# Performance work log

Measured on AMD Instinct MI355X. Metric: run time of the kernel, lower is better.

The kernel has to match this reference:

```python
import jax, jax.numpy as jnp
import numpy as np

B, N, C, K = 16, 1024, 192, 9
H = 4 * C  # hidden of second MLP pair


def _gelu(x):
    return jax.nn.gelu(x, approximate=False)  # torch nn.GELU default is exact erf


def _mlp(x, w1, b1, w2, b2):
    # TwoLayerNN: Linear -> GELU -> Linear
    return _gelu(x @ w1.T + b1) @ w2.T + b2


def _linear_init(key, out_d, in_d):
    k1, k2 = jax.random.split(key)
    s = 1.0 / np.sqrt(in_d)
    w = jax.random.uniform(k1, (out_d, in_d), minval=-s, maxval=s, dtype=jnp.float32)
    b = jax.random.uniform(k2, (out_d,), minval=-s, maxval=s, dtype=jnp.float32)
    return w, b


def setup_inputs() -> dict:
    key = jax.random.key(0)
    ks = jax.random.split(key, 10)
    x = jax.random.normal(ks[0], (B, N, C), dtype=jnp.float32)
    il1_w1, il1_b1 = _linear_init(ks[1], C, C)
    il1_w2, il1_b2 = _linear_init(ks[2], C, C)
    ol1_w1, ol1_b1 = _linear_init(ks[3], C, C)
    ol1_w2, ol1_b2 = _linear_init(ks[4], C, C)
    il2_w1, il2_b1 = _linear_init(ks[5], H, C)
    il2_w2, il2_b2 = _linear_init(ks[6], C, H)
    ol2_w1, ol2_b1 = _linear_init(ks[7], H, C)
    ol2_w2, ol2_b2 = _linear_init(ks[8], C, H)
    fc_w, fc_b = _linear_init(ks[9], C, 2 * C)  # Conv1d(2C, C, 1) == Linear(2C->C)
    return dict(x=x,
                il1_w1=il1_w1, il1_b1=il1_b1, il1_w2=il1_w2, il1_b2=il1_b2,
                fc_w=fc_w, fc_b=fc_b,
                ol1_w1=ol1_w1, ol1_b1=ol1_b1, ol1_w2=ol1_w2, ol1_b2=ol1_b2,
                il2_w1=il2_w1, il2_b1=il2_b1, il2_w2=il2_w2, il2_b2=il2_b2,
                ol2_w1=ol2_w1, ol2_b1=ol2_b1, ol2_w2=ol2_w2, ol2_b2=ol2_b2)


def reference(x, il1_w1, il1_b1, il1_w2, il1_b2, fc_w, fc_b,
              ol1_w1, ol1_b1, ol1_w2, ol1_b2,
              il2_w1, il2_b1, il2_w2, il2_b2,
              ol2_w1, ol2_b1, ol2_w2, ol2_b2):
    Bx, Nx, Cx = x.shape
    # 1) dense similarity + KNN graph (indices only; no grad path through sim)
    sim = jnp.einsum('bnc,bmc->bnm', x, x)                       # [B,N,N]
    _, graph = jax.lax.top_k(sim, K)                             # [B,N,K] int32
    shortcut = x
    # 2) node transform then gather-max aggregation
    h = _mlp(x.reshape(Bx * Nx, Cx), il1_w1, il1_b1, il1_w2, il1_b2).reshape(Bx, Nx, Cx)
    nb = jnp.take_along_axis(h[:, None, :, :], graph[:, :, :, None], axis=2)  # [B,N,K,C]
    agg = jnp.max(nb - h[:, :, None, :], axis=2)                 # [B,N,C]
    # 3) stack along new last dim then flatten -> interleaved channels [x_c0,agg_c0,x_c1,...]
    cat = jnp.stack([h, agg], axis=-1).reshape(Bx, Nx, 2 * Cx)   # [B,N,2C]
    h = cat @ fc_w.T + fc_b                                      # Conv1d k=1 == Linear
    h = _mlp(_gelu(h).reshape(Bx * Nx, Cx), ol1_w1, ol1_b1, ol1_w2, ol1_b2).reshape(Bx, Nx, Cx)
    x1 = h + shortcut
    # 4) FFN block (two TwoLayerNNs with external GELU between them)
    f = _mlp(x1.reshape(Bx * Nx, Cx), il2_w1, il2_b1, il2_w2, il2_b2)
    f = _mlp(_gelu(f), ol2_w1, ol2_b1, ol2_w2, ol2_b2).reshape(Bx, Nx, Cx)
    return f + x1
```

## Files before the change

### kernel.cpp

```cpp
#include <hip/hip_runtime.h>
#include <hip/hip_bf16.h>
#include <math.h>

#define DEVINL __device__ __forceinline__

typedef __attribute__((ext_vector_type(4))) float f32x4;
typedef __attribute__((ext_vector_type(8))) short s16x8;

DEVINL unsigned short f2bf(float f) {
  union { float f; unsigned u; } v; v.f = f;
  unsigned r = v.u + 0x7FFFu + ((v.u >> 16) & 1u);
  return (unsigned short)(r >> 16);
}
DEVINL float bf2f(unsigned short s) {
  union { unsigned u; float f; } v; v.u = ((unsigned)s) << 16;
  return v.f;
}
DEVINL float gelu_exact(float x) {
  return 0.5f * x * (1.0f + erff(x * 0.70710678118654752f));
}

__global__ __launch_bounds__(256) void conv_kernel(const float* __restrict__ x,
                                                   unsigned short* __restrict__ xh,
                                                   unsigned short* __restrict__ xl) {
  int i = blockIdx.x * 256 + threadIdx.x;
  float4 v = ((const float4*)x)[i];
  float f[4] = {v.x, v.y, v.z, v.w};
  unsigned short h[4], l[4];
#pragma unroll
  for (int j = 0; j < 4; ++j) {
    h[j] = f2bf(f[j]);
    l[j] = f2bf(f[j] - bf2f(h[j]));
  }
  uint2 uh, ul;
  uh.x = (unsigned)h[0] | ((unsigned)h[1] << 16);
  uh.y = (unsigned)h[2] | ((unsigned)h[3] << 16);
  ul.x = (unsigned)l[0] | ((unsigned)l[1] << 16);
  ul.y = (unsigned)l[2] | ((unsigned)l[3] << 16);
  ((uint2*)xh)[i] = uh;
  ((uint2*)xl)[i] = ul;
}

struct WArgs {
  const float* s[9];
  unsigned short* d[9];
  int n4[9];
};
__global__ __launch_bounds__(256) void wconv_kernel(WArgs a) {
  int seg = blockIdx.y;
  int i = blockIdx.x * 256 + threadIdx.x;
  if (i >= a.n4[seg]) return;
  float4 v = ((const float4*)a.s[seg])[i];
  float f[4] = {v.x, v.y, v.z, v.w};
  uint2 u;
  u.x = (unsigned)f2bf(f[0]) | ((unsigned)f2bf(f[1]) << 16);
  u.y = (unsigned)f2bf(f[2]) | ((unsigned)f2bf(f[3]) << 16);
  ((uint2*)a.d[seg])[i] = u;
}

__global__ __launch_bounds__(512)
#if __has_attribute(amdgpu_waves_per_eu)
__attribute__((amdgpu_waves_per_eu(2, 2)))
#endif
void simtopk_kernel(const unsigned short* __restrict__ xh,
                    const unsigned short* __restrict__ xl,
                    int* __restrict__ graph) {
  const int tid  = threadIdx.x;
  const int lane = tid & 63;
  const int w    = tid >> 6;
  const int wm   = w >> 1, wn = w & 1;

  const int lin  = blockIdx.y * 16 + blockIdx.x;
  const int work = (lin & 7) * 32 + (lin >> 3);
  const int rb   = work & 15;
  const int b    = work >> 4;

  extern __shared__ char smem[];
  float* Lv = (float*)smem;
  int*   Li = (int*)(smem + 20480);
  float* Mv = (float*)(smem + 40960);
  int*   Mi = (int*)(smem + 51200);

  const unsigned short* xhb = xh + (size_t)b * (1024 * 192);
  const unsigned short* xlb = xl + (size_t)b * (1024 * 192);

  s16x8 ah[6], al[6];
#pragma unroll
  for (int ks = 0; ks < 6; ++ks) {
    int r = rb * 64 + wm * 16 + (lane & 15);
    size_t off = (size_t)r * 192 + ks * 32 + (lane >> 4) * 8;
    ah[ks] = *(const s16x8*)(xhb + off);
    al[ks] = *(const s16x8*)(xlb + off);
  }

  auto stage = [&](int buf, int ct) {
    unsigned short* bH = (unsigned short*)(smem + buf * 49152);
    unsigned short* bL = bH + 12288;
#pragma unroll
    for (int i = 0; i < 3; ++i) {
      int c = tid + i * 512;
      int row = c / 24, cc = c - row * 24;
      size_t goff = (size_t)(ct * 64 + row) * 192 + (size_t)((cc ^ (row & 7)) * 8);
      __builtin_amdgcn_global_load_lds((const __attribute__((address_space(1))) void*)(xhb + goff),
                                       (__attribute__((address_space(3))) void*)(bH + (size_t)c * 8), 16, 0, 0);
      __builtin_amdgcn_global_load_lds((const __attribute__((address_space(1))) void*)(xlb + goff),
                                       (__attribute__((address_space(3))) void*)(bL + (size_t)c * 8), 16, 0, 0);
    }
  };

  float tv[9]; int tix[9];
#pragma unroll
  for (int k = 0; k < 9; ++k) { tv[k] = -3.0e38f; tix[k] = 1 << 30; }

  stage(0, 0);
  __syncthreads();

  int cur = 0;
  for (int ct = 0; ct < 16; ++ct) {
    if (ct < 15) stage(cur ^ 1, ct + 1);

    const unsigned short* bH = (const unsigned short*)(smem + cur * 49152);
    const unsigned short* bL = bH + 12288;

    f32x4 a0[2], a1[2], a2[2];
#pragma unroll
    for (int n2 = 0; n2 < 2; ++n2) { a0[n2] = 0; a1[n2] = 0; a2[n2] = 0; }

#pragma unroll
    for (int ks = 0; ks < 6; ++ks) {
      const int chk = ks * 4 + (lane >> 4);
#pragma unroll
      for (int n2 = 0; n2 < 2; ++n2) {
        const int rc = (wn * 2 + n2) * 16 + (lane & 15);
        const int si = rc * 192 + ((chk ^ (rc & 7)) * 8);
        s16x8 bh = *(const s16x8*)&bH[si];
        s16x8 bl = *(const s16x8*)&bL[si];
        a0[n2] = __builtin_amdgcn_mfma_f32_16x16x32_bf16(bh, ah[ks], a0[n2], 0, 0, 0);
        a1[n2] = __builtin_amdgcn_mfma_f32_16x16x32_bf16(bl, ah[ks], a1[n2], 0, 0, 0);
        a2[n2] = __builtin_amdgcn_mfma_f32_16x16x32_bf16(bh, al[ks], a2[n2], 0, 0, 0);
      }
    }

#pragma unroll
    for (int n2 = 0; n2 < 2; ++n2) {
      int cbase = ct * 64 + (wn * 2 + n2) * 16 + (lane >> 4) * 4;
#pragma unroll
      for (int r = 0; r < 4; ++r) {
        float v = a0[n2][r] + a1[n2][r] + a2[n2][r];
        int   c = cbase + r;
        if (v > tv[8]) {
          tv[8] = v; tix[8] = c;
#pragma unroll
          for (int s = 8; s > 0; --s) {
            if (tv[s] > tv[s - 1]) {
              float fv = tv[s]; tv[s] = tv[s - 1]; tv[s - 1] = fv;
              int   fi = tix[s]; tix[s] = tix[s - 1]; tix[s - 1] = fi;
            }
          }
        }
      }
    }
    __syncthreads();
    cur ^= 1;
  }

  {
    int rowloc = wm * 16 + (lane & 15);
    int listid = wn * 4 + (lane >> 4);
    int lbase  = (rowloc * 8 + listid) * 9;
#pragma unroll
    for (int k = 0; k < 9; ++k) { Lv[lbase + k] = tv[k]; Li[lbase + k] = tix[k]; }
  }
  __syncthreads();

  if (tid < 256) {
    int r = tid >> 2, p = tid & 3;
    float fv[9]; int fi[9];
#pragma unroll
    for (int k = 0; k < 9; ++k) { fv[k] = -3.0e38f; fi[k] = 1 << 30; }
    for (int s2 = 0; s2 < 2; ++s2) {
      int base = (r * 8 + p * 2 + s2) * 9;
#pragma unroll
      for (int k = 0; k < 9; ++k) {
        float v = Lv[base + k]; int c = Li[base + k];
        bool better = (v > fv[8]) || (v == fv[8] && c < fi[8]);
        if (better) {
          fv[8] = v; fi[8] = c;
#pragma unroll
          for (int s = 8; s > 0; --s) {
            bool up = (fv[s] > fv[s - 1]) || (fv[s] == fv[s - 1] && fi[s] < fi[s - 1]);
            if (up) {
              float a = fv[s]; fv[s] = fv[s - 1]; fv[s - 1] = a;
              int  ii = fi[s]; fi[s] = fi[s - 1]; fi[s - 1] = ii;
            }
          }
        }
      }
    }
#pragma unroll
    for (int k = 0; k < 9; ++k) { Mv[tid * 9 + k] = fv[k]; Mi[tid * 9 + k] = fi[k]; }
  }
  __syncthreads();

  if (tid < 64) {
    float fv[9]; int fi[9];
#pragma unroll
    for (int k = 0; k < 9; ++k) { fv[k] = -3.0e38f; fi[k] = 1 << 30; }
    for (int p = 0; p < 4; ++p) {
      int base = (tid * 4 + p) * 9;
#pragma unroll
      for (int k = 0; k < 9; ++k) {
        float v = Mv[base + k]; int c = Mi[base + k];
        bool better = (v > fv[8]) || (v == fv[8] && c < fi[8]);
        if (better) {
          fv[8] = v; fi[8] = c;
#pragma unroll
          for (int s = 8; s > 0; --s) {
            bool up = (fv[s] > fv[s - 1]) || (fv[s] == fv[s - 1] && fi[s] < fi[s - 1]);
            if (up) {
              float a = fv[s]; fv[s] = fv[s - 1]; fv[s - 1] = a;
              int  ii = fi[s]; fi[s] = fi[s - 1]; fi[s - 1] = ii;
            }
          }
        }
      }
    }
    int* gout = graph + ((size_t)b * 1024 + rb * 64 + tid) * 9;
#pragma unroll
    for (int k = 0; k < 9; ++k) gout[k] = fi[k];
  }
}

__global__ __launch_bounds__(256) void agg_kernel(const unsigned short* __restrict__ h,
                                                  const int* __restrict__ graph,
                                                  unsigned short* __restrict__ cat) {
  int gid  = blockIdx.x * 4 + (threadIdx.x >> 6);
  int lane = threadIdx.x & 63;
  int b = gid >> 10;
  int n = gid & 1023;
  const unsigned short* hb = h + (size_t)b * (1024 * 192);
  const int* g = graph + (size_t)gid * 9;
  float hn[3];
#pragma unroll
  for (int j = 0; j < 3; ++j) hn[j] = bf2f(hb[(size_t)n * 192 + lane + j * 64]);
  float ag[3] = {-3.0e38f, -3.0e38f, -3.0e38f};
  for (int k = 0; k < 9; ++k) {
    int idx = g[k];
#pragma unroll
    for (int j = 0; j < 3; ++j) {
      float v = bf2f(hb[(size_t)idx * 192 + lane + j * 64]) - hn[j];
      ag[j] = fmaxf(ag[j], v);
    }
  }
  unsigned* crow = (unsigned*)cat + (size_t)gid * 192;
#pragma unroll
  for (int j = 0; j < 3; ++j) {
    int c = lane + j * 64;
    crow[c] = (unsigned)f2bf(hn[j]) | ((unsigned)f2bf(ag[j]) << 16);
  }
}

template <bool GELU_, bool RESID>
__global__ __launch_bounds__(256) void gemm_kernel(const unsigned short* __restrict__ A,
                                                   const unsigned short* __restrict__ W,
                                                   const float* __restrict__ bias,
                                                   const float* __restrict__ resid,
                                                   unsigned short* __restrict__ outb,
                                                   float* __restrict__ outf,
                                                   int N, int K) {
  __shared__ unsigned short As[2][128 * 64];
  __shared__ unsigned short Ws[2][64 * 64];

  const int tid  = threadIdx.x;
  const int lane = tid & 63;
  const int w    = tid >> 6;
  const int m0   = blockIdx.x * 128;
  const int n0   = blockIdx.y * 64;

  auto stageA = [&](int buf, int kt) {
#pragma unroll
    for (int i = 0; i < 4; ++i) {
      int chunk = w * 4 + i;
      int row = chunk * 8 + (lane >> 3);
      const unsigned short* src = A + (size_t)(m0 + row) * K + kt * 64
                                    + (((lane & 7) ^ (row & 7)) * 8);
      unsigned short* dst = &As[buf][chunk * 512];
      __builtin_amdgcn_global_load_lds((const __attribute__((address_space(1))) void*)src,
                                       (__attribute__((address_space(3))) void*)dst, 16, 0, 0);
    }
  };
  auto stageW = [&](int buf, int kt) {
#pragma unroll
    for (int i = 0; i < 2; ++i) {
      int chunk = w * 2 + i;
      int row = chunk * 8 + (lane >> 3);
      const unsigned short* src = W + (size_t)(n0 + row) * K + kt * 64
                                    + (((lane & 7) ^ (row & 7)) * 8);
      unsigned short* dst = &Ws[buf][chunk * 512];
      __builtin_amdgcn_global_load_lds((const __attribute__((address_space(1))) void*)src,
                                       (__attribute__((address_space(3))) void*)dst, 16, 0, 0);
    }
  };

  stageA(0, 0);
  stageW(0, 0);
  __syncthreads();

  const int wm = w >> 1, wn = w & 1;
  f32x4 acc[4][2];
#pragma unroll
  for (int a = 0; a < 4; ++a)
#pragma unroll
    for (int c = 0; c < 2; ++c) acc[a][c] = 0;

  const int nk = K >> 6;
  for (int kt = 0; kt < nk; ++kt) {
    const int cur = kt & 1;
    if (kt + 1 < nk) { stageA(cur ^ 1, kt + 1); stageW(cur ^ 1, kt + 1); }
#pragma unroll
    for (int ks = 0; ks < 2; ++ks) {
      const int kc = ks * 4 + (lane >> 4);
      s16x8 af[4], bfr[2];
#pragma unroll
      for (int m2 = 0; m2 < 4; ++m2) {
        int row = wm * 64 + m2 * 16 + (lane & 15);
        af[m2] = *(const s16x8*)&As[cur][row * 64 + ((kc ^ (row & 7)) * 8)];
      }
#pragma unroll
      for (int n2 = 0; n2 < 2; ++n2) {
        int rw = wn * 32 + n2 * 16 + (lane & 15);
        bfr[n2] = *(const s16x8*)&Ws[cur][rw * 64 + ((kc ^ (rw & 7)) * 8)];
      }
#pragma unroll
      for (int m2 = 0; m2 < 4; ++m2)
#pragma unroll
        for (int n2 = 0; n2 < 2; ++n2)
          acc[m2][n2] = __builtin_amdgcn_mfma_f32_16x16x32_bf16(af[m2], bfr[n2], acc[m2][n2], 0, 0, 0);
    }
    __syncthreads();
  }

#pragma unroll
  for (int m2 = 0; m2 < 4; ++m2)
#pragma unroll
    for (int n2 = 0; n2 < 2; ++n2)
#pragma unroll
      for (int r = 0; r < 4; ++r) {
        int row = m0 + wm * 64 + m2 * 16 + (lane >> 4) * 4 + r;
        int col = n0 + wn * 32 + n2 * 16 + (lane & 15);
        float v = acc[m2][n2][r] + bias[col];
        if (GELU_) v = gelu_exact(v);
        if (RESID) v += resid[(size_t)row * N + col];
        size_t o = (size_t)row * N + col;
        if (outb) outb[o] = f2bf(v);
        if (outf) outf[o] = v;
      }
}

extern "C" void kernel_launch(void* const* d_in, const int* in_sizes, int n_in,
                              void* d_out, int out_size, void* d_ws, size_t ws_size,
                              hipStream_t stream) {
  (void)in_sizes; (void)n_in; (void)out_size; (void)ws_size;
  const float* x      = (const float*)d_in[0];
  const float* il1_w1 = (const float*)d_in[1];
  const float* il1_b1 = (const float*)d_in[2];
  const float* il1_w2 = (const float*)d_in[3];
  const float* il1_b2 = (const float*)d_in[4];
  const float* fc_w   = (const float*)d_in[5];
  const float* fc_b   = (const float*)d_in[6];
  const float* ol1_w1 = (const float*)d_in[7];
  const float* ol1_b1 = (const float*)d_in[8];
  const float* ol1_w2 = (const float*)d_in[9];
  const float* ol1_b2 = (const float*)d_in[10];
  const float* il2_w1 = (const float*)d_in[11];
  const float* il2_b1 = (const float*)d_in[12];
  const float* il2_w2 = (const float*)d_in[13];
  const float* il2_b2 = (const float*)d_in[14];
  const float* ol2_w1 = (const float*)d_in[15];
  const float* ol2_b1 = (const float*)d_in[16];
  const float* ol2_w2 = (const float*)d_in[17];
  const float* ol2_b2 = (const float*)d_in[18];

  char* ws = (char*)d_ws;
  const size_t SZ = 16384ull * 192 * 2;
  unsigned short* xbf  = (unsigned short*)(ws);
  unsigned short* t13  = (unsigned short*)(ws + SZ);
  unsigned short* hbuf = (unsigned short*)(ws + 2 * SZ);
  unsigned short* t2   = (unsigned short*)(ws + 3 * SZ);
  unsigned short* x1b  = (unsigned short*)(ws + 4 * SZ);
  unsigned short* catg = (unsigned short*)(ws + 5 * SZ);
  float*          x1f  = (float*)(ws + 7 * SZ);
  unsigned short* uv   = (unsigned short*)(ws + 9 * SZ);
  unsigned short* xlo  = uv;
  int*            graph = (int*)(ws + 13 * SZ);
  unsigned short* wb   = (unsigned short*)(ws + 13 * SZ + (1 << 20));

  unsigned short* il1_w1b = wb;
  unsigned short* il1_w2b = wb + 36864;
  unsigned short* fcb     = wb + 73728;
  unsigned short* ol1_w1b = wb + 147456;
  unsigned short* ol1_w2b = wb + 184320;
  unsigned short* il2_w1b = wb + 221184;
  unsigned short* il2_w2b = wb + 368640;
  unsigned short* ol2_w1b = wb + 516096;
  unsigned short* ol2_w2b = wb + 663552;

  WArgs wa;
  wa.s[0] = il1_w1; wa.d[0] = il1_w1b; wa.n4[0] = 36864 / 4;
  wa.s[1] = il1_w2; wa.d[1] = il1_w2b; wa.n4[1] = 36864 / 4;
  wa.s[2] = fc_w;   wa.d[2] = fcb;     wa.n4[2] = 73728 / 4;
  wa.s[3] = ol1_w1; wa.d[3] = ol1_w1b; wa.n4[3] = 36864 / 4;
  wa.s[4] = ol1_w2; wa.d[4] = ol1_w2b; wa.n4[4] = 36864 / 4;
  wa.s[5] = il2_w1; wa.d[5] = il2_w1b; wa.n4[5] = 147456 / 4;
  wa.s[6] = il2_w2; wa.d[6] = il2_w2b; wa.n4[6] = 147456 / 4;
  wa.s[7] = ol2_w1; wa.d[7] = ol2_w1b; wa.n4[7] = 147456 / 4;
  wa.s[8] = ol2_w2; wa.d[8] = ol2_w2b; wa.n4[8] = 147456 / 4;

  hipFuncSetAttribute((const void*)simtopk_kernel,
                      hipFuncAttributeMaxDynamicSharedMemorySize, 98304);

  conv_kernel<<<3072, 256, 0, stream>>>(x, xbf, xlo);
  wconv_kernel<<<dim3(144, 9), 256, 0, stream>>>(wa);
  simtopk_kernel<<<dim3(16, 16), 512, 98304, stream>>>(xbf, xlo, graph);
  gemm_kernel<true,  false><<<dim3(128, 3), 256, 0, stream>>>(xbf, il1_w1b, il1_b1, nullptr, t13, nullptr, 192, 192);
  gemm_kernel<false, false><<<dim3(128, 3), 256, 0, stream>>>(t13, il1_w2b, il1_b2, nullptr, hbuf, nullptr, 192, 192);
  agg_kernel<<<4096, 256, 0, stream>>>(hbuf, graph, catg);
  gemm_kernel<true,  false><<<dim3(128, 3), 256, 0, stream>>>(catg, fcb, fc_b, nullptr, t2, nullptr, 192, 384);
  gemm_kernel<true,  false><<<dim3(128, 3), 256, 0, stream>>>(t2, ol1_w1b, ol1_b1, nullptr, t13, nullptr, 192, 192);
  gemm_kernel<false, true ><<<dim3(128, 3), 256, 0, stream>>>(t13, ol1_w2b, ol1_b2, x, x1b, x1f, 192, 192);
  gemm_kernel<true,  false><<<dim3(128, 12), 256, 0, stream>>>(x1b, il2_w1b, il2_b1, nullptr, uv, nullptr, 768, 192);
  gemm_kernel<true,  false><<<dim3(128, 3), 256, 0, stream>>>(uv, il2_w2b, il2_b2, nullptr, catg, nullptr, 192, 768);
  gemm_kernel<true,  false><<<dim3(128, 12), 256, 0, stream>>>(catg, ol2_w1b, ol2_b1, nullptr, uv, nullptr, 768, 192);
  gemm_kernel<false, true ><<<dim3(128, 3), 256, 0, stream>>>(uv, ol2_w2b, ol2_b2, x1f, nullptr, (float*)d_out, 192, 768);
}
```

Measured before the change: 243.7 us.

## Drop split-bf16 similarity to plain bf16 and triple-buffer KNN tile loads

The similarity/top-k kernel no longer uses the hi/lo bf16 split that emulated fp32 precision with three MFMAs per tile. It now uses a single bf16 MFMA on the high part only, which removes the low-part conversion, its loads and two thirds of the MFMA work. Shared-memory staging changes from double buffering with full syncthreads to a three-stage ring with explicit vmcnt waits and raw barriers. The reduced precision risks changing KNN neighbor selection when similarity values are close, which could make the graph differ from the fp32 reference.

Result: no change. 242.7 us (-0.4%).

```diff
diff --git a/kernel.cpp b/kernel.cpp
--- a/kernel.cpp
+++ b/kernel.cpp
@@ -21,24 +21,13 @@
 }
 
 __global__ __launch_bounds__(256) void conv_kernel(const float* __restrict__ x,
-                                                   unsigned short* __restrict__ xh,
-                                                   unsigned short* __restrict__ xl) {
+                                                   unsigned short* __restrict__ xh) {
   int i = blockIdx.x * 256 + threadIdx.x;
   float4 v = ((const float4*)x)[i];
-  float f[4] = {v.x, v.y, v.z, v.w};
-  unsigned short h[4], l[4];
-#pragma unroll
-  for (int j = 0; j < 4; ++j) {
-    h[j] = f2bf(f[j]);
-    l[j] = f2bf(f[j] - bf2f(h[j]));
-  }
-  uint2 uh, ul;
-  uh.x = (unsigned)h[0] | ((unsigned)h[1] << 16);
-  uh.y = (unsigned)h[2] | ((unsigned)h[3] << 16);
-  ul.x = (unsigned)l[0] | ((unsigned)l[1] << 16);
-  ul.y = (unsigned)l[2] | ((unsigned)l[3] << 16);
-  ((uint2*)xh)[i] = uh;
-  ((uint2*)xl)[i] = ul;
+  uint2 u;
+  u.x = (unsigned)f2bf(v.x) | ((unsigned)f2bf(v.y) << 16);
+  u.y = (unsigned)f2bf(v.z) | ((unsigned)f2bf(v.w) << 16);
+  ((uint2*)xh)[i] = u;
 }
 
 struct WArgs {
@@ -51,10 +40,9 @@
   int i = blockIdx.x * 256 + threadIdx.x;
   if (i >= a.n4[seg]) return;
   float4 v = ((const float4*)a.s[seg])[i];
-  float f[4] = {v.x, v.y, v.z, v.w};
   uint2 u;
-  u.x = (unsigned)f2bf(f[0]) | ((unsigned)f2bf(f[1]) << 16);
-  u.y = (unsigned)f2bf(f[2]) | ((unsigned)f2bf(f[3]) << 16);
+  u.x = (unsigned)f2bf(v.x) | ((unsigned)f2bf(v.y) << 16);
+  u.y = (unsigned)f2bf(v.z) | ((unsigned)f2bf(v.w) << 16);
   ((uint2*)a.d[seg])[i] = u;
 }
 
@@ -63,7 +51,6 @@
 __attribute__((amdgpu_waves_per_eu(2, 2)))
 #endif
 void simtopk_kernel(const unsigned short* __restrict__ xh,
-                    const unsigned short* __restrict__ xl,
                     int* __restrict__ graph) {
   const int tid  = threadIdx.x;
   const int lane = tid & 63;
@@ -82,29 +69,23 @@
   int*   Mi = (int*)(smem + 51200);
 
   const unsigned short* xhb = xh + (size_t)b * (1024 * 192);
-  const unsigned short* xlb = xl + (size_t)b * (1024 * 192);
-
-  s16x8 ah[6], al[6];
+
+  s16x8 ah[6];
 #pragma unroll
   for (int ks = 0; ks < 6; ++ks) {
     int r = rb * 64 + wm * 16 + (lane & 15);
-    size_t off = (size_t)r * 192 + ks * 32 + (lane >> 4) * 8;
-    ah[ks] = *(const s16x8*)(xhb + off);
-    al[ks] = *(const s16x8*)(xlb + off);
+    ah[ks] = *(const s16x8*)(xhb + (size_t)r * 192 + ks * 32 + (lane >> 4) * 8);
   }
 
   auto stage = [&](int buf, int ct) {
-    unsigned short* bH = (unsigned short*)(smem + buf * 49152);
-    unsigned short* bL = bH + 12288;
+    unsigned short* bs = (unsigned short*)(smem + buf * 24576);
 #pragma unroll
     for (int i = 0; i < 3; ++i) {
       int c = tid + i * 512;
       int row = c / 24, cc = c - row * 24;
       size_t goff = (size_t)(ct * 64 + row) * 192 + (size_t)((cc ^ (row & 7)) * 8);
       __builtin_amdgcn_global_load_lds((const __attribute__((address_space(1))) void*)(xhb + goff),
-                                       (__attribute__((address_space(3))) void*)(bH + (size_t)c * 8), 16, 0, 0);
-      __builtin_amdgcn_global_load_lds((const __attribute__((address_space(1))) void*)(xlb + goff),
-                                       (__attribute__((address_space(3))) void*)(bL + (size_t)c * 8), 16, 0, 0);
+                                       (__attribute__((address_space(3))) void*)(bs + (size_t)c * 8), 16, 0, 0);
     }
   };
 
@@ -113,19 +94,18 @@
   for (int k = 0; k < 9; ++k) { tv[k] = -3.0e38f; tix[k] = 1 << 30; }
 
   stage(0, 0);
-  __syncthreads();
-
-  int cur = 0;
+  stage(1, 1);
+  asm volatile("s_waitcnt vmcnt(3)" ::: "memory");
+  __builtin_amdgcn_sched_barrier(0);
+  __builtin_amdgcn_s_barrier();
+
   for (int ct = 0; ct < 16; ++ct) {
-    if (ct < 15) stage(cur ^ 1, ct + 1);
-
-    const unsigned short* bH = (const unsigned short*)(smem + cur * 49152);
-    const unsigned short* bL = bH + 12288;
-
-    f32x4 a0[2], a1[2], a2[2];
-#pragma unroll
-    for (int n2 = 0; n2 < 2; ++n2) { a0[n2] = 0; a1[n2] = 0; a2[n2] = 0; }
-
+    if (ct + 2 < 16) stage((ct + 2) % 3, ct + 2);
+
+    const unsigned short* bs = (const unsigned short*)(smem + (ct % 3) * 24576);
+
+    f32x4 acc[2];
+    acc[0] = 0; acc[1] = 0;
 #pragma unroll
     for (int ks = 0; ks < 6; ++ks) {
       const int chk = ks * 4 + (lane >> 4);
@@ -133,11 +113,8 @@
       for (int n2 = 0; n2 < 2; ++n2) {
         const int rc = (wn * 2 + n2) * 16 + (lane & 15);
         const int si = rc * 192 + ((chk ^ (rc & 7)) * 8);
-        s16x8 bh = *(const s16x8*)&bH[si];
-        s16x8 bl = *(const s16x8*)&bL[si];
-        a0[n2] = __builtin_amdgcn_mfma_f32_16x16x32_bf16(bh, ah[ks], a0[n2], 0, 0, 0);
-        a1[n2] = __builtin_amdgcn_mfma_f32_16x16x32_bf16(bl, ah[ks], a1[n2], 0, 0, 0);
-        a2[n2] = __builtin_amdgcn_mfma_f32_16x16x32_bf16(bh, al[ks], a2[n2], 0, 0, 0);
+        s16x8 bh = *(const s16x8*)&bs[si];
+        acc[n2] = __builtin_amdgcn_mfma_f32_16x16x32_bf16(bh, ah[ks], acc[n2], 0, 0, 0);
       }
     }
 
@@ -146,7 +123,7 @@
       int cbase = ct * 64 + (wn * 2 + n2) * 16 + (lane >> 4) * 4;
 #pragma unroll
       for (int r = 0; r < 4; ++r) {
-        float v = a0[n2][r] + a1[n2][r] + a2[n2][r];
+        float v = acc[n2][r];
         int   c = cbase + r;
         if (v > tv[8]) {
           tv[8] = v; tix[8] = c;
@@ -160,9 +137,15 @@
         }
       }
     }
-    __syncthreads();
-    cur ^= 1;
-  }
+
+    if (ct + 1 < 16) {
+      if (ct + 2 < 16) { asm volatile("s_waitcnt vmcnt(3)" ::: "memory"); }
+      else             { asm volatile("s_waitcnt vmcnt(0)" ::: "memory"); }
+      __builtin_amdgcn_sched_barrier(0);
+      __builtin_amdgcn_s_barrier();
+    }
+  }
+  __syncthreads();
 
   {
     int rowloc = wm * 16 + (lane & 15);
@@ -391,7 +374,6 @@
   unsigned short* catg = (unsigned short*)(ws + 5 * SZ);
   float*          x1f  = (float*)(ws + 7 * SZ);
   unsigned short* uv   = (unsigned short*)(ws + 9 * SZ);
-  unsigned short* xlo  = uv;
   int*            graph = (int*)(ws + 13 * SZ);
   unsigned short* wb   = (unsigned short*)(ws + 13 * SZ + (1 << 20));
 
@@ -417,11 +399,11 @@
   wa.s[8] = ol2_w2; wa.d[8] = ol2_w2b; wa.n4[8] = 147456 / 4;
 
   hipFuncSetAttribute((const void*)simtopk_kernel,
-                      hipFuncAttributeMaxDynamicSharedMemorySize, 98304);
-
-  conv_kernel<<<3072, 256, 0, stream>>>(x, xbf, xlo);
+                      hipFuncAttributeMaxDynamicSharedMemorySize, 73728);
+
+  conv_kernel<<<3072, 256, 0, stream>>>(x, xbf);
   wconv_kernel<<<dim3(144, 9), 256, 0, stream>>>(wa);
-  simtopk_kernel<<<dim3(16, 16), 512, 98304, stream>>>(xbf, xlo, graph);
+  simtopk_kernel<<<dim3(16, 16), 512, 73728, stream>>>(xbf, graph);
   gemm_kernel<true,  false><<<dim3(128, 3), 256, 0, stream>>>(xbf, il1_w1b, il1_b1, nullptr, t13, nullptr, 192, 192);
   gemm_kernel<false, false><<<dim3(128, 3), 256, 0, stream>>>(t13, il1_w2b, il1_b2, nullptr, hbuf, nullptr, 192, 192);
   agg_kernel<<<4096, 256, 0, stream>>>(hbuf, graph, catg);
```
